# Kernel optimization log

Hardware: AMD Instinct MI355X
Metric: run time of the kernel (lower is better)

## Reference

```python
import jax, jax.numpy as jnp
import numpy as np

B, S, E, H = 4, 2048, 1024, 16
D = E // H  # head_dim = 64


def setup_inputs() -> dict:
    key = jax.random.key(0)
    ks = jax.random.split(key, 9)
    scale = 1.0 / np.sqrt(E)
    return {
        "x": jax.random.normal(ks[0], (B, S, E), dtype=jnp.float32),
        "Wq": jax.random.normal(ks[1], (E, E), dtype=jnp.float32) * scale,
        "bq": jax.random.normal(ks[2], (E,), dtype=jnp.float32) * 0.01,
        "Wk": jax.random.normal(ks[3], (E, E), dtype=jnp.float32) * scale,
        "bk": jax.random.normal(ks[4], (E,), dtype=jnp.float32) * 0.01,
        "Wv": jax.random.normal(ks[5], (E, E), dtype=jnp.float32) * scale,
        "bv": jax.random.normal(ks[6], (E,), dtype=jnp.float32) * 0.01,
        "Wo": jax.random.normal(ks[7], (E, E), dtype=jnp.float32) * scale,
        "bo": jax.random.normal(ks[8], (E,), dtype=jnp.float32) * 0.01,
    }


def reference(x, Wq, bq, Wk, bk, Wv, bv, Wo, bo):
    b, s, e = x.shape
    # Linear projections (torch Linear: y = x @ W.T + b), split into heads: [b, h, s, d]
    def proj(W, bias):
        return (x @ W.T + bias).reshape(b, s, H, D).transpose(0, 2, 1, 3)

    q = proj(Wq, bq)
    k = proj(Wk, bk)
    v = proj(Wv, bv)

    # scores: [b, h, s, s], scaled by 1/sqrt(head_dim)
    scores = jnp.einsum("bhqd,bhkd->bhqk", q, k) / jnp.sqrt(jnp.float32(D))
    probs = jax.nn.softmax(scores, axis=-1)
    # dropout_rate=0.0 -> identity

    # weighted values: [b, h, s, d] -> [b, s, e]
    out = jnp.einsum("bhqk,bhkd->bhqd", probs, v)
    out = out.transpose(0, 2, 1, 3).reshape(b, s, e)
    return out @ Wo.T + bo
```

## Files before the change

kernel.cpp:

```cpp
#include <hip/hip_runtime.h>
#include <hip/hip_bf16.h>
#include <math.h>

#define B_ 4
#define S_ 2048
#define E_ 1024
#define H_ 16
#define D_ 64
#define MTOT (B_ * S_)

typedef __attribute__((ext_vector_type(8))) short short8;
typedef __attribute__((ext_vector_type(4))) float f32x4;
typedef __attribute__((ext_vector_type(16))) float f32x16;
typedef unsigned short u16;
typedef unsigned int u32;

static __device__ __forceinline__ u16 bfbits(float x) {
  __hip_bfloat16 h = __float2bfloat16(x);
  return *reinterpret_cast<u16*>(&h);
}
static __device__ __forceinline__ u32 pk2(float a, float b) {
  return (u32)bfbits(a) | ((u32)bfbits(b) << 16);
}

static __device__ __forceinline__ void gload_lds16(const void* g, void* l) {
  __builtin_amdgcn_global_load_lds(
      (const __attribute__((address_space(1))) u32*)g,
      (__attribute__((address_space(3))) u32*)l, 16, 0, 0);
}

static __device__ __forceinline__ void plane_swap(u32& a, u32& b) {
#if __has_builtin(__builtin_amdgcn_permlane32_swap)
  auto r = __builtin_amdgcn_permlane32_swap(a, b, false, false);
  a = r[0];
  b = r[1];
#else
  const u32 as = __shfl_xor(a, 32);
  const u32 bs = __shfl_xor(b, 32);
  const int hi = (threadIdx.x & 63) >> 5;
  const u32 na = hi ? bs : a;
  const u32 nb = hi ? b : as;
  a = na;
  b = nb;
#endif
}

__global__ __launch_bounds__(256) void f2bf(const float* __restrict__ in,
                                            u16* __restrict__ out, int n4) {
  int i = blockIdx.x * blockDim.x + threadIdx.x;
  const int stride = gridDim.x * blockDim.x;
  for (; i < n4; i += stride) {
    const float4 v = reinterpret_cast<const float4*>(in)[i];
    ushort4 o;
    o.x = bfbits(v.x); o.y = bfbits(v.y); o.z = bfbits(v.z); o.w = bfbits(v.w);
    reinterpret_cast<ushort4*>(out)[i] = o;
  }
}

template <int MODE>
__global__ __launch_bounds__(256) void gemm_bf16(
    const u16* __restrict__ A, const u16* __restrict__ Bw,
    const float* __restrict__ bias, void* __restrict__ outp,
    int M, int N, int K, float alpha) {
  __shared__ u16 As[128 * 32];
  __shared__ u16 Bs[128 * 32];

  const int tid = threadIdx.x;
  const int lane = tid & 63;
  const int w = tid >> 6;
  const int wr = w >> 1, wc = w & 1;
  const int m0 = blockIdx.y << 7, n0 = blockIdx.x << 7;
  const int l15 = lane & 15, l4 = lane >> 4;

  f32x4 acc[4][4];
#pragma unroll
  for (int i = 0; i < 4; ++i)
#pragma unroll
    for (int j = 0; j < 4; ++j) {
      f32x4 z = {0.f, 0.f, 0.f, 0.f};
      acc[i][j] = z;
    }

  const int srow = w << 5;
  const u16* Ag = A + (size_t)(m0 + srow + (lane >> 2)) * K + ((lane & 3) << 3);
  const u16* Bg = Bw + (size_t)(n0 + srow + (lane >> 2)) * K + ((lane & 3) << 3);
  u16* AsW = As + srow * 32;
  u16* BsW = Bs + srow * 32;
  const size_t rstep = (size_t)16 * K;

  const u16* Afrag = As + ((wr << 6) + l15) * 32 + (l4 << 3);
  const u16* Bfrag = Bs + ((wc << 6) + l15) * 32 + (l4 << 3);

  for (int k0 = 0; k0 < K; k0 += 32) {
    gload_lds16(Ag + k0, AsW);
    gload_lds16(Ag + rstep + k0, AsW + 512);
    gload_lds16(Bg + k0, BsW);
    gload_lds16(Bg + rstep + k0, BsW + 512);
    __syncthreads();
    short8 a[4], b[4];
#pragma unroll
    for (int i = 0; i < 4; ++i) a[i] = *(const short8*)(Afrag + i * 512);
#pragma unroll
    for (int j = 0; j < 4; ++j) b[j] = *(const short8*)(Bfrag + j * 512);
#pragma unroll
    for (int i = 0; i < 4; ++i)
#pragma unroll
      for (int j = 0; j < 4; ++j)
        acc[i][j] = __builtin_amdgcn_mfma_f32_16x16x32_bf16(a[i], b[j],
                                                            acc[i][j], 0, 0, 0);
    __syncthreads();
  }

  const int mbase = m0 + (wr << 6);
  const int nbase = n0 + (wc << 6);

  if (MODE == 0) {
    u16* out = (u16*)outp;
#pragma unroll
    for (int ni = 0; ni < 4; ++ni) {
      const int n = nbase + ni * 16 + l15;
      const int hh = n >> 6, d = n & 63;
      const float bn = bias[n];
#pragma unroll
      for (int mi = 0; mi < 4; ++mi)
#pragma unroll
        for (int r = 0; r < 4; ++r) {
          const int m = mbase + mi * 16 + (l4 << 2) + r;
          const int bb = m >> 11, s = m & (S_ - 1);
          const float v = (acc[mi][ni][r] + bn) * alpha;
          out[(((size_t)(bb * H_ + hh) * S_ + s) << 6) + d] = bfbits(v);
        }
    }
  } else if (MODE == 1) {
    u16* out = (u16*)outp;
#pragma unroll
    for (int mi = 0; mi < 4; ++mi)
#pragma unroll
      for (int r = 0; r < 4; ++r) {
        const int m = mbase + mi * 16 + (l4 << 2) + r;
        const float bm = bias[m];
#pragma unroll
        for (int ni = 0; ni < 4; ++ni) {
          const int n = nbase + ni * 16 + l15;
          out[(size_t)m * N + n] = bfbits(acc[mi][ni][r] + bm);
        }
      }
  } else {
    float* out = (float*)outp;
#pragma unroll
    for (int ni = 0; ni < 4; ++ni) {
      const int n = nbase + ni * 16 + l15;
      const float bn = bias[n];
#pragma unroll
      for (int mi = 0; mi < 4; ++mi)
#pragma unroll
        for (int r = 0; r < 4; ++r) {
          const int m = mbase + mi * 16 + (l4 << 2) + r;
          out[(size_t)m * N + n] = acc[mi][ni][r] + bn;
        }
    }
  }
}

__global__ __launch_bounds__(256) void attn_mfma2(
    const u16* __restrict__ Q, const u16* __restrict__ K,
    const u16* __restrict__ Vt, u16* __restrict__ out) {
  __shared__ u16 Ks[2][64 * 64];
  __shared__ u16 Vs[2][64 * 64];
  __shared__ u16 Ep[4][32 * 72];

  const int tid = threadIdx.x;
  const int lane = tid & 63;
  const int w = tid >> 6;
  const int l31 = lane & 31, hi = lane >> 5;
  const int bh = blockIdx.y;
  const int b = bh >> 4, h = bh & 15;
  const int q0 = blockIdx.x << 7;
  const int qw = q0 + (w << 5);

  const u16* Qg = Q + ((size_t)bh * S_ + qw + l31) * D_ + (hi << 3);
  short8 qf[4];
#pragma unroll
  for (int ks = 0; ks < 4; ++ks) qf[ks] = *(const short8*)(Qg + (ks << 4));

  f32x16 o0, o1;
#pragma unroll
  for (int u = 0; u < 16; ++u) { o0[u] = 0.f; o1[u] = 0.f; }
  float m_r = -3e38f, l_r = 0.f;

  const int rr = lane >> 3;
  const int cs = (lane & 7) ^ rr;
  const u16* Kg = K + ((size_t)bh * S_ + (w << 4) + rr) * D_ + (cs << 3);
  const u16* Vg = Vt + ((size_t)((h << 6) + (w << 4) + rr)) * MTOT +
                  (size_t)b * S_ + (cs << 3);

#define STAGE(bufi, kt)                                   \
  do {                                                    \
    u16* kd = Ks[bufi] + ((w << 4) << 6);                 \
    u16* vd = Vs[bufi] + ((w << 4) << 6);                 \
    gload_lds16(Kg + (size_t)(kt)*D_, kd);                \
    gload_lds16(Kg + (size_t)((kt) + 8) * D_, kd + 512);  \
    gload_lds16(Vg + (kt), vd);                           \
    gload_lds16(Vg + (size_t)8 * MTOT + (kt), vd + 512);  \
  } while (0)

  STAGE(0, 0);
  __syncthreads();

  for (int t = 0; t < S_ / 64; ++t) {
    const int cur = t & 1;
    if (t + 1 < S_ / 64) STAGE(cur ^ 1, (t + 1) << 6);

    const u16* KsB = Ks[cur];
    const u16* VsB = Vs[cur];

    f32x16 s0, s1;
#pragma unroll
    for (int u = 0; u < 16; ++u) { s0[u] = 0.f; s1[u] = 0.f; }
    __builtin_amdgcn_s_setprio(1);
#pragma unroll
    for (int ks = 0; ks < 4; ++ks) {
      const int ch = (((ks << 1) + hi) ^ (l31 & 7)) << 3;
      const short8 k0 = *(const short8*)&KsB[(l31 << 6) + ch];
      const short8 k1 = *(const short8*)&KsB[((32 + l31) << 6) + ch];
      s0 = __builtin_amdgcn_mfma_f32_32x32x16_bf16(k0, qf[ks], s0, 0, 0, 0);
      s1 = __builtin_amdgcn_mfma_f32_32x32x16_bf16(k1, qf[ks], s1, 0, 0, 0);
    }
    __builtin_amdgcn_s_setprio(0);

    float t16[16];
#pragma unroll
    for (int u = 0; u < 16; ++u) t16[u] = fmaxf(s0[u], s1[u]);
#pragma unroll
    for (int st = 8; st > 0; st >>= 1)
#pragma unroll
      for (int u = 0; u < 16; ++u)
        if (u < st) t16[u] = fmaxf(t16[u], t16[u + st]);
    float hm = fmaxf(t16[0], __shfl_xor(t16[0], 32));
    const float mn = fmaxf(m_r, hm);
    const float corr = exp2f(m_r - mn);
    m_r = mn;
#pragma unroll
    for (int u = 0; u < 16; ++u) {
      s0[u] = exp2f(s0[u] - mn);
      s1[u] = exp2f(s1[u] - mn);
    }
    float a16[16];
#pragma unroll
    for (int u = 0; u < 16; ++u) a16[u] = s0[u] + s1[u];
#pragma unroll
    for (int st = 8; st > 0; st >>= 1)
#pragma unroll
      for (int u = 0; u < 16; ++u)
        if (u < st) a16[u] += a16[u + st];
    float rs = a16[0] + __shfl_xor(a16[0], 32);
    l_r = l_r * corr + rs;
#pragma unroll
    for (int u = 0; u < 16; ++u) { o0[u] *= corr; o1[u] *= corr; }

    short8 pf[4];
#pragma unroll
    for (int ks2 = 0; ks2 < 4; ++ks2) {
      const int ub = (ks2 << 3) & 15;
#define EV(u) (((ks2 << 3) + (u)) < 16 ? s0 : s1)[(ub + (u)) & 15]
      u32 a0 = pk2(EV(0), EV(1));
      u32 a0b = pk2(EV(2), EV(3));
      u32 a1 = pk2(EV(4), EV(5));
      u32 a1b = pk2(EV(6), EV(7));
#undef EV
      plane_swap(a0, a1);
      plane_swap(a0b, a1b);
      union { u32 wd[4]; short8 v; } pu;
      pu.wd[0] = a0; pu.wd[1] = a0b; pu.wd[2] = a1; pu.wd[3] = a1b;
      pf[ks2] = pu.v;
    }

    __builtin_amdgcn_s_setprio(1);
#pragma unroll
    for (int ks2 = 0; ks2 < 4; ++ks2) {
      const int ch = (((ks2 << 1) + hi) ^ (l31 & 7)) << 3;
      const short8 v0 = *(const short8*)&VsB[(l31 << 6) + ch];
      const short8 v1 = *(const short8*)&VsB[((32 + l31) << 6) + ch];
      o0 = __builtin_amdgcn_mfma_f32_32x32x16_bf16(v0, pf[ks2], o0, 0, 0, 0);
      o1 = __builtin_amdgcn_mfma_f32_32x32x16_bf16(v1, pf[ks2], o1, 0, 0, 0);
    }
    __builtin_amdgcn_s_setprio(0);
    __syncthreads();
  }

  const float inv = 1.f / l_r;
  u16* ep = Ep[w];
#pragma unroll
  for (int t2 = 0; t2 < 2; ++t2) {
#pragma unroll
    for (int reg = 0; reg < 16; reg += 2) {
      const int d = (t2 << 5) + ((reg >> 2) << 3) + (hi << 2) + (reg & 3);
      const float x0 = (t2 ? o1[reg] : o0[reg]) * inv;
      const float x1 = (t2 ? o1[reg + 1] : o0[reg + 1]) * inv;
      *(u32*)&ep[l31 * 72 + d] = pk2(x0, x1);
    }
  }
#pragma unroll
  for (int pass = 0; pass < 4; ++pass) {
    const int row = (pass << 3) + (lane >> 3);
    const short8 t8 = *(const short8*)&ep[row * 72 + ((lane & 7) << 3)];
    *(short8*)(out + ((size_t)(b * S_ + q0 + (w << 5) + row)) * E_ + (h << 6) +
               ((lane & 7) << 3)) = t8;
  }
}

extern "C" void kernel_launch(void* const* d_in, const int* in_sizes, int n_in,
                              void* d_out, int out_size, void* d_ws,
                              size_t ws_size, hipStream_t stream) {
  const float* x  = (const float*)d_in[0];
  const float* Wq = (const float*)d_in[1];
  const float* bq = (const float*)d_in[2];
  const float* Wk = (const float*)d_in[3];
  const float* bk = (const float*)d_in[4];
  const float* Wv = (const float*)d_in[5];
  const float* bv = (const float*)d_in[6];
  const float* Wo = (const float*)d_in[7];
  const float* bo = (const float*)d_in[8];

  u16* wsp = (u16*)d_ws;
  const size_t nx = (size_t)MTOT * E_;
  const size_t nw = (size_t)E_ * E_;
  u16* xb  = wsp;
  u16* wqb = xb + nx;
  u16* wkb = wqb + nw;
  u16* wvb = wkb + nw;
  u16* wob = wvb + nw;
  u16* qb  = wob + nw;
  u16* kb  = qb + nx;
  u16* vtb = kb + nx;
  u16* ab  = vtb + nx;

  const dim3 blk(256);

  hipLaunchKernelGGL(f2bf, dim3(2048), blk, 0, stream, x, xb, (int)(nx / 4));
  hipLaunchKernelGGL(f2bf, dim3(512), blk, 0, stream, Wq, wqb, (int)(nw / 4));
  hipLaunchKernelGGL(f2bf, dim3(512), blk, 0, stream, Wk, wkb, (int)(nw / 4));
  hipLaunchKernelGGL(f2bf, dim3(512), blk, 0, stream, Wv, wvb, (int)(nw / 4));
  hipLaunchKernelGGL(f2bf, dim3(512), blk, 0, stream, Wo, wob, (int)(nw / 4));

  const float qscale = 0.125f * 1.4426950408889634f;

  hipLaunchKernelGGL((gemm_bf16<0>), dim3(E_ / 128, MTOT / 128), blk, 0, stream,
                     xb, wqb, bq, qb, MTOT, E_, E_, qscale);
  hipLaunchKernelGGL((gemm_bf16<0>), dim3(E_ / 128, MTOT / 128), blk, 0, stream,
                     xb, wkb, bk, kb, MTOT, E_, E_, 1.0f);
  hipLaunchKernelGGL((gemm_bf16<1>), dim3(MTOT / 128, E_ / 128), blk, 0, stream,
                     wvb, xb, bv, vtb, E_, MTOT, E_, 1.0f);
  hipLaunchKernelGGL(attn_mfma2, dim3(S_ / 128, B_ * H_), blk, 0, stream,
                     qb, kb, vtb, ab);
  hipLaunchKernelGGL((gemm_bf16<2>), dim3(E_ / 128, MTOT / 128), blk, 0, stream,
                     ab, wob, bo, d_out, MTOT, E_, E_, 1.0f);
}
```

Measured before the change: 378.9 us.

## Add lazy softmax rescaling, alias LDS buffers, swizzle attention epilogue

The attention kernel now skips the running-max update and the rescaling of the output accumulators whenever every lane's new tile max stays within 8 (log2 units) of the current max. Values stay exact because the final divide by l_r cancels the shift. The kernel also reuses the K/V shared memory pool for the epilogue staging buffer, which cuts LDS use and may allow more blocks per CU. It XOR-swizzles the epilogue writes and reads to reduce bank conflicts. Finally, it seeds the first QK MFMA with a zero vector instead of zeroing the score registers each iteration, and replaces the tree max-reduction with a linear chain. The trade-off is a wave-wide vote and a branch per tile, and P values up to 256 before the bf16 conversion.

```diff
diff --git a/kernel.cpp b/kernel.cpp
--- a/kernel.cpp
+++ b/kernel.cpp
@@ -162,12 +162,12 @@
   }
 }
 
-__global__ __launch_bounds__(256) void attn_mfma2(
+__global__ __launch_bounds__(256) void attn_mfma3(
     const u16* __restrict__ Q, const u16* __restrict__ K,
     const u16* __restrict__ Vt, u16* __restrict__ out) {
-  __shared__ u16 Ks[2][64 * 64];
-  __shared__ u16 Vs[2][64 * 64];
-  __shared__ u16 Ep[4][32 * 72];
+  __shared__ u16 pool[16384];
+  u16* Ksb = pool;
+  u16* Vsb = pool + 8192;
 
   const int tid = threadIdx.x;
   const int lane = tid & 63;
@@ -183,9 +183,9 @@
 #pragma unroll
   for (int ks = 0; ks < 4; ++ks) qf[ks] = *(const short8*)(Qg + (ks << 4));
 
-  f32x16 o0, o1;
-#pragma unroll
-  for (int u = 0; u < 16; ++u) { o0[u] = 0.f; o1[u] = 0.f; }
+  f32x16 o0, o1, fz;
+#pragma unroll
+  for (int u = 0; u < 16; ++u) { o0[u] = 0.f; o1[u] = 0.f; fz[u] = 0.f; }
   float m_r = -3e38f, l_r = 0.f;
 
   const int rr = lane >> 3;
@@ -196,8 +196,8 @@
 
 #define STAGE(bufi, kt)                                   \
   do {                                                    \
-    u16* kd = Ks[bufi] + ((w << 4) << 6);                 \
-    u16* vd = Vs[bufi] + ((w << 4) << 6);                 \
+    u16* kd = Ksb + (bufi)*4096 + (w << 10);              \
+    u16* vd = Vsb + (bufi)*4096 + (w << 10);              \
     gload_lds16(Kg + (size_t)(kt)*D_, kd);                \
     gload_lds16(Kg + (size_t)((kt) + 8) * D_, kd + 512);  \
     gload_lds16(Vg + (kt), vd);                           \
@@ -211,15 +211,20 @@
     const int cur = t & 1;
     if (t + 1 < S_ / 64) STAGE(cur ^ 1, (t + 1) << 6);
 
-    const u16* KsB = Ks[cur];
-    const u16* VsB = Vs[cur];
+    const u16* KsB = Ksb + cur * 4096;
+    const u16* VsB = Vsb + cur * 4096;
 
     f32x16 s0, s1;
-#pragma unroll
-    for (int u = 0; u < 16; ++u) { s0[u] = 0.f; s1[u] = 0.f; }
     __builtin_amdgcn_s_setprio(1);
-#pragma unroll
-    for (int ks = 0; ks < 4; ++ks) {
+    {
+      const int ch = (hi ^ (l31 & 7)) << 3;
+      const short8 k0 = *(const short8*)&KsB[(l31 << 6) + ch];
+      const short8 k1 = *(const short8*)&KsB[((32 + l31) << 6) + ch];
+      s0 = __builtin_amdgcn_mfma_f32_32x32x16_bf16(k0, qf[0], fz, 0, 0, 0);
+      s1 = __builtin_amdgcn_mfma_f32_32x32x16_bf16(k1, qf[0], fz, 0, 0, 0);
+    }
+#pragma unroll
+    for (int ks = 1; ks < 4; ++ks) {
       const int ch = (((ks << 1) + hi) ^ (l31 & 7)) << 3;
       const short8 k0 = *(const short8*)&KsB[(l31 << 6) + ch];
       const short8 k1 = *(const short8*)&KsB[((32 + l31) << 6) + ch];
@@ -231,15 +236,18 @@
     float t16[16];
 #pragma unroll
     for (int u = 0; u < 16; ++u) t16[u] = fmaxf(s0[u], s1[u]);
-#pragma unroll
-    for (int st = 8; st > 0; st >>= 1)
-#pragma unroll
-      for (int u = 0; u < 16; ++u)
-        if (u < st) t16[u] = fmaxf(t16[u], t16[u + st]);
-    float hm = fmaxf(t16[0], __shfl_xor(t16[0], 32));
-    const float mn = fmaxf(m_r, hm);
-    const float corr = exp2f(m_r - mn);
-    m_r = mn;
+    float tm = fmaxf(t16[0], t16[1]);
+#pragma unroll
+    for (int u = 2; u + 1 < 16; u += 2) tm = fmaxf(fmaxf(tm, t16[u]), t16[u + 1]);
+    const float hm = fmaxf(tm, __shfl_xor(tm, 32));
+
+    const bool skip = __all(hm <= m_r + 8.f);
+    float mn = m_r, corr = 1.f;
+    if (!skip) {
+      mn = fmaxf(m_r, hm);
+      corr = exp2f(m_r - mn);
+      m_r = mn;
+    }
 #pragma unroll
     for (int u = 0; u < 16; ++u) {
       s0[u] = exp2f(s0[u] - mn);
@@ -253,10 +261,14 @@
 #pragma unroll
       for (int u = 0; u < 16; ++u)
         if (u < st) a16[u] += a16[u + st];
-    float rs = a16[0] + __shfl_xor(a16[0], 32);
-    l_r = l_r * corr + rs;
-#pragma unroll
-    for (int u = 0; u < 16; ++u) { o0[u] *= corr; o1[u] *= corr; }
+    const float rs = a16[0] + __shfl_xor(a16[0], 32);
+    if (skip) {
+      l_r += rs;
+    } else {
+      l_r = l_r * corr + rs;
+#pragma unroll
+      for (int u = 0; u < 16; ++u) { o0[u] *= corr; o1[u] *= corr; }
+    }
 
     short8 pf[4];
 #pragma unroll
@@ -289,23 +301,27 @@
   }
 
   const float inv = 1.f / l_r;
-  u16* ep = Ep[w];
+  u16* ep = pool + w * 2304;
+  const int g = l31 >> 3;
 #pragma unroll
   for (int t2 = 0; t2 < 2; ++t2) {
 #pragma unroll
     for (int reg = 0; reg < 16; reg += 2) {
       const int d = (t2 << 5) + ((reg >> 2) << 3) + (hi << 2) + (reg & 3);
+      const int ds = (((d >> 3) ^ g) << 3) | (d & 7);
       const float x0 = (t2 ? o1[reg] : o0[reg]) * inv;
       const float x1 = (t2 ? o1[reg + 1] : o0[reg + 1]) * inv;
-      *(u32*)&ep[l31 * 72 + d] = pk2(x0, x1);
-    }
-  }
+      *(u32*)&ep[l31 * 72 + ds] = pk2(x0, x1);
+    }
+  }
+  __builtin_amdgcn_s_waitcnt(0);
 #pragma unroll
   for (int pass = 0; pass < 4; ++pass) {
     const int row = (pass << 3) + (lane >> 3);
-    const short8 t8 = *(const short8*)&ep[row * 72 + ((lane & 7) << 3)];
+    const int cc = lane & 7;
+    const short8 t8 = *(const short8*)&ep[row * 72 + ((cc ^ pass) << 3)];
     *(short8*)(out + ((size_t)(b * S_ + q0 + (w << 5) + row)) * E_ + (h << 6) +
-               ((lane & 7) << 3)) = t8;
+               (cc << 3)) = t8;
   }
 }
 
@@ -351,7 +367,7 @@
                      xb, wkb, bk, kb, MTOT, E_, E_, 1.0f);
   hipLaunchKernelGGL((gemm_bf16<1>), dim3(MTOT / 128, E_ / 128), blk, 0, stream,
                      wvb, xb, bv, vtb, E_, MTOT, E_, 1.0f);
-  hipLaunchKernelGGL(attn_mfma2, dim3(S_ / 128, B_ * H_), blk, 0, stream,
+  hipLaunchKernelGGL(attn_mfma3, dim3(S_ / 128, B_ * H_), blk, 0, stream,
                      qb, kb, vtb, ab);
   hipLaunchKernelGGL((gemm_bf16<2>), dim3(E_ / 128, MTOT / 128), blk, 0, stream,
                      ab, wob, bo, d_out, MTOT, E_, E_, 1.0f);
```

Result: faster. 370.2 us (-2.3%).
